# Kernel tuning notes

Hardware: AMD Instinct MI355X
Metric: run time of the kernel (lower is better)

## Reference

```python
import jax, jax.numpy as jnp
import numpy as np

B, T, Hs, Ws, D, NH, NKV = 2, 8, 16, 16, 1024, 16, 4
HD = D // NH  # 64
EPS = 1e-6
THETA = 10000.0


def setup_inputs() -> dict:
    key = jax.random.key(0)
    ks = jax.random.split(key, 6)
    N = T * Hs * Ws
    s = 0.02
    return {
        'x': jax.random.normal(ks[0], (B, N, D), jnp.float32),
        'Wq': jax.random.normal(ks[1], (D, D), jnp.float32) * s,
        'bq': jnp.zeros((D,), jnp.float32),
        'Wk': jax.random.normal(ks[2], (D, NKV * HD), jnp.float32) * s,
        'bk': jnp.zeros((NKV * HD,), jnp.float32),
        'Wv': jax.random.normal(ks[3], (D, NKV * HD), jnp.float32) * s,
        'bv': jnp.zeros((NKV * HD,), jnp.float32),
        'Wo': jax.random.normal(ks[4], (D, D), jnp.float32) * s,
        'bo': jnp.zeros((D,), jnp.float32),
        'qn_w': jnp.ones((HD,), jnp.float32),
        'kn_w': jnp.ones((HD,), jnp.float32),
        't': T, 'h': Hs, 'w': Ws,
    }


def _rms_norm(x, w):
    # RMSNorm over last dim (head_dim), eps=1e-6, learned scale
    var = jnp.mean(jnp.square(x), axis=-1, keepdims=True)
    return x * jax.lax.rsqrt(var + EPS) * w


def _rope_cs(n, d):
    inv = 1.0 / (THETA ** (np.arange(0, d, 2, dtype=np.float32) / d))
    fr = np.arange(n, dtype=np.float32)[:, None] * inv[None, :]
    emb = np.concatenate([fr, fr], axis=-1)  # (n, d)
    return jnp.asarray(np.cos(emb)), jnp.asarray(np.sin(emb))


def _rot_half(x):
    x1, x2 = jnp.split(x, 2, axis=-1)
    return jnp.concatenate([-x2, x1], axis=-1)


def _st_rope(x, t, h, w):
    # x: (B, t, h, w, heads, hd); factored 3D RoPE on head_dim split
    d = x.shape[-1]
    if d % 3 == 0:
        dt = dh = d // 3
        dw = d - 2 * dt
    else:
        dt = d // 4
        dh = d // 4
        dw = d - dt - dh
    xt, xh, xw = jnp.split(x, [dt, dt + dh], axis=-1)

    def app(xs, n, axis_pos, dd):
        cos, sin = _rope_cs(n, dd)
        shp = [1] * 6
        shp[axis_pos] = n
        shp[-1] = dd
        cos = cos.reshape(shp)
        sin = sin.reshape(shp)
        return xs * cos + _rot_half(xs) * sin

    xt = app(xt, t, 1, dt)
    xh = app(xh, h, 2, dh)
    xw = app(xw, w, 3, dw)
    return jnp.concatenate([xt, xh, xw], axis=-1)


def reference(x, Wq, bq, Wk, bk, Wv, bv, Wo, bo, qn_w, kn_w, t, h, w):
    Bx, N, Dx = x.shape
    q = (x @ Wq + bq).reshape(Bx, N, NH, HD)
    k = (x @ Wk + bk).reshape(Bx, N, NKV, HD)
    v = (x @ Wv + bv).reshape(Bx, N, NKV, HD)
    q = _rms_norm(q, qn_w)
    k = _rms_norm(k, kn_w)
    q = _st_rope(q.reshape(Bx, t, h, w, NH, HD), t, h, w).reshape(Bx, N, NH, HD)
    k = _st_rope(k.reshape(Bx, t, h, w, NKV, HD), t, h, w).reshape(Bx, N, NKV, HD)
    g = NH // NKV
    if g > 1:  # GQA: 'b m h d -> b m (h g) d'
        k = jnp.repeat(k, g, axis=2)
        v = jnp.repeat(v, g, axis=2)
    scale = HD ** -0.5
    scores = jnp.einsum('bnhd,bmhd->bhnm', q, k) * scale  # (B,H,N,N)
    p = jax.nn.softmax(scores, axis=-1)
    out = jnp.einsum('bhnm,bmhd->bnhd', p, v).reshape(Bx, N, Dx)
    return out @ Wo + bo
```

## Files before the change

kernel.cpp:

```cpp
#include <hip/hip_runtime.h>
#include <hip/hip_bf16.h>
#include <math.h>

constexpr int B_   = 2;
constexpr int N_   = 2048;
constexpr int D_   = 1024;
constexpr int NH_  = 16;
constexpr int NKV_ = 4;
constexpr int HD_  = 64;
constexpr int BN_  = 4096;
constexpr int KVD_ = NKV_ * HD_;
constexpr float EPS_ = 1e-6f;
constexpr float THETA_ = 10000.0f;

typedef _Float16 half8v __attribute__((ext_vector_type(8)));
typedef unsigned short ushort8v __attribute__((ext_vector_type(8)));
typedef float f32x4 __attribute__((ext_vector_type(4)));

static __device__ __forceinline__ unsigned short f2h(float f) {
  union { _Float16 h; unsigned short u; } v; v.h = (_Float16)f; return v.u;
}
static __device__ __forceinline__ float h2f(unsigned short u) {
  union { unsigned short u; _Float16 h; } v; v.u = u; return (float)v.h;
}

static __device__ __forceinline__ void dma16(const unsigned short* g,
                                             unsigned short* l) {
  __builtin_amdgcn_global_load_lds(
      (const __attribute__((address_space(1))) unsigned int*)g,
      (__attribute__((address_space(3))) unsigned int*)l, 16, 0, 0);
}

static __device__ __forceinline__ void wtrans_tile(
    const float* __restrict__ W, int Nw, int K, float scale,
    unsigned short* __restrict__ WTh, unsigned short* __restrict__ WTl,
    int bx, int by, bool lo)
{
  __shared__ float tile[32][33];
  const int k0 = bx * 32, n0 = by * 32;
  const int c = threadIdx.x & 31, rb = threadIdx.x >> 5;
#pragma unroll
  for (int i = 0; i < 4; ++i) {
    const int r = rb + i * 8;
    tile[r][c] = W[(size_t)(k0 + r) * Nw + n0 + c];
  }
  __syncthreads();
#pragma unroll
  for (int i = 0; i < 4; ++i) {
    const int r = rb + i * 8;
    const float v = tile[c][r] * scale;
    const size_t o = (size_t)(n0 + r) * K + k0 + c;
    const unsigned short hi = f2h(v);
    WTh[o] = hi;
    if (lo) WTl[o] = f2h(v - h2f(hi));
  }
}

__global__ __launch_bounds__(256) void prep(
    const float* __restrict__ x,
    const float* __restrict__ Wq, const float* __restrict__ Wk,
    const float* __restrict__ Wv, const float* __restrict__ Wo,
    unsigned short* __restrict__ xh,
    unsigned short* __restrict__ WqT, unsigned short* __restrict__ WkT,
    unsigned short* __restrict__ WvT,
    unsigned short* __restrict__ WoTh, unsigned short* __restrict__ WoTl)
{
  const int bid = blockIdx.x;
  if (bid < 2048) {
    const int i = (bid * 256 + threadIdx.x) * 8;
    const float4 v0 = *(const float4*)(x + i);
    const float4 v1 = *(const float4*)(x + i + 4);
    ushort8v o;
    o[0] = f2h(v0.x); o[1] = f2h(v0.y); o[2] = f2h(v0.z); o[3] = f2h(v0.w);
    o[4] = f2h(v1.x); o[5] = f2h(v1.y); o[6] = f2h(v1.z); o[7] = f2h(v1.w);
    *(ushort8v*)(xh + i) = o;
  } else if (bid < 3072) {
    const int l = bid - 2048;
    wtrans_tile(Wq, D_, D_, 1.0f, WqT, nullptr, l & 31, l >> 5, false);
  } else if (bid < 3328) {
    const int l = bid - 3072;
    wtrans_tile(Wk, KVD_, D_, 1.0f, WkT, nullptr, l & 31, l >> 5, false);
  } else if (bid < 3584) {
    const int l = bid - 3328;
    wtrans_tile(Wv, KVD_, D_, 1.0f, WvT, nullptr, l & 31, l >> 5, false);
  } else {
    const int l = bid - 3584;
    wtrans_tile(Wo, D_, D_, 64.0f, WoTh, WoTl, l & 31, l >> 5, true);
  }
}

__global__ __launch_bounds__(256) void gemm_qkv(
    const unsigned short* __restrict__ xh,
    const unsigned short* __restrict__ WqT, const unsigned short* __restrict__ WkT,
    const unsigned short* __restrict__ WvT,
    const float* __restrict__ bq, const float* __restrict__ bk, const float* __restrict__ bv,
    const float* __restrict__ qn, const float* __restrict__ kn,
    unsigned short* __restrict__ qv, unsigned short* __restrict__ kv,
    unsigned short* __restrict__ vv)
{
  __shared__ unsigned short As[128 * 64];
  __shared__ unsigned short Bs[64 * 64];

  const int y = blockIdx.y;
  const unsigned short* wt; const float* bias; unsigned short* outp; int opitch, col0, mode;
  if (y < 16)      { wt = WqT + (size_t)y * 64 * D_;        bias = bq + y * 64;        outp = qv; opitch = D_;   col0 = y * 64;        mode = 0; }
  else if (y < 20) { wt = WkT + (size_t)(y - 16) * 64 * D_; bias = bk + (y - 16) * 64; outp = kv; opitch = KVD_; col0 = (y - 16) * 64; mode = 1; }
  else             { wt = WvT + (size_t)(y - 20) * 64 * D_; bias = bv + (y - 20) * 64; outp = vv; opitch = KVD_; col0 = (y - 20) * 64; mode = 2; }

  const int bm = blockIdx.x * 128;
  const int tid = threadIdx.x;
  const int w = tid >> 6, lane = tid & 63, quad = lane >> 4, l16 = lane & 15;
  const int lr = lane >> 3;
  const int gc = (lane & 7) ^ lr;
  const int sw = l16 & 7;

  const unsigned short* gA = xh + (size_t)(bm + w * 8 + lr) * D_ + gc * 8;
  const unsigned short* gB = wt + (size_t)(w * 8 + lr) * D_ + gc * 8;

  f32x4 acc[2][4];
#pragma unroll
  for (int i = 0; i < 2; ++i)
#pragma unroll
    for (int j = 0; j < 4; ++j) acc[i][j] = (f32x4){0.f, 0.f, 0.f, 0.f};

  for (int k0 = 0; k0 < D_; k0 += 64) {
    __syncthreads();
#pragma unroll
    for (int rd = 0; rd < 4; ++rd)
      dma16(gA + (size_t)rd * 32 * D_ + k0, &As[rd * 2048 + w * 512]);
#pragma unroll
    for (int rd = 0; rd < 2; ++rd)
      dma16(gB + (size_t)rd * 32 * D_ + k0, &Bs[rd * 2048 + w * 512]);
    __syncthreads();

#pragma unroll
    for (int kk = 0; kk < 2; ++kk) {
      half8v fa[2], fb[4];
#pragma unroll
      for (int mb = 0; mb < 2; ++mb)
        fa[mb] = *(const half8v*)&As[(w * 32 + mb * 16 + l16) * 64 + ((kk * 4 + quad) ^ sw) * 8];
#pragma unroll
      for (int nb = 0; nb < 4; ++nb)
        fb[nb] = *(const half8v*)&Bs[(nb * 16 + l16) * 64 + ((kk * 4 + quad) ^ sw) * 8];
#pragma unroll
      for (int mb = 0; mb < 2; ++mb)
#pragma unroll
        for (int nb = 0; nb < 4; ++nb)
          acc[mb][nb] = __builtin_amdgcn_mfma_f32_16x16x32_f16(fa[mb], fb[nb], acc[mb][nb], 0, 0, 0);
    }
  }

  float bsv[4];
#pragma unroll
  for (int nb = 0; nb < 4; ++nb) bsv[nb] = bias[nb * 16 + l16];

  if (mode == 2) {
#pragma unroll
    for (int mb = 0; mb < 2; ++mb)
#pragma unroll
      for (int nb = 0; nb < 4; ++nb)
#pragma unroll
        for (int r = 0; r < 4; ++r) {
          const int row = bm + w * 32 + mb * 16 + quad * 4 + r;
          outp[(size_t)row * opitch + col0 + nb * 16 + l16] = f2h(acc[mb][nb][r] + bsv[nb]);
        }
    return;
  }

  const float* nwp = (mode == 0) ? qn : kn;
  float wv[4];
#pragma unroll
  for (int nb = 0; nb < 4; ++nb) wv[nb] = nwp[nb * 16 + l16];
  const float f_th = __powf(THETA_, -(float)(l16 & 7) / 8.0f);
  const float f_w  = __powf(THETA_, -(float)l16 / 16.0f);
  const float oscale = (mode == 0) ? 0.125f : 1.0f;
  const bool first8 = (l16 & 8) == 0;

  float snw[4], csw[4];
#pragma unroll
  for (int r = 0; r < 4; ++r)
    __sincosf((float)(quad * 4 + r) * f_w, &snw[r], &csw[r]);

#pragma unroll
  for (int mb = 0; mb < 2; ++mb) {
    const int nbase = (bm + w * 32 + mb * 16) & (N_ - 1);
    float snt, cst, snh, csh;
    __sincosf((float)(nbase >> 8) * f_th, &snt, &cst);
    __sincosf((float)((nbase >> 4) & 15) * f_th, &snh, &csh);
#pragma unroll
    for (int r = 0; r < 4; ++r) {
      float v[4];
      float ss = 0.f;
#pragma unroll
      for (int nb = 0; nb < 4; ++nb) { v[nb] = acc[mb][nb][r] + bsv[nb]; ss += v[nb] * v[nb]; }
      ss += __shfl_xor(ss, 1, 64);
      ss += __shfl_xor(ss, 2, 64);
      ss += __shfl_xor(ss, 4, 64);
      ss += __shfl_xor(ss, 8, 64);
      const float rs = rsqrtf(ss * (1.0f / 64.0f) + EPS_);
#pragma unroll
      for (int nb = 0; nb < 4; ++nb) v[nb] *= rs * wv[nb];

      const float p0 = __shfl_xor(v[0], 8, 64);
      const float p1 = __shfl_xor(v[1], 8, 64);
      const float o0 = v[0] * cst + (first8 ? -p0 : p0) * snt;
      const float o1 = v[1] * csh + (first8 ? -p1 : p1) * snh;
      const float o2 = v[2] * csw[r] - v[3] * snw[r];
      const float o3 = v[3] * csw[r] + v[2] * snw[r];

      const int row = bm + w * 32 + mb * 16 + quad * 4 + r;
      const size_t ob = (size_t)row * opitch + col0 + l16;
      outp[ob]      = f2h(o0 * oscale);
      outp[ob + 16] = f2h(o1 * oscale);
      outp[ob + 32] = f2h(o2 * oscale);
      outp[ob + 48] = f2h(o3 * oscale);
    }
  }
}

__global__ __launch_bounds__(256) void gemm_o(
    const unsigned short* __restrict__ ag,
    const unsigned short* __restrict__ WTh, const unsigned short* __restrict__ WTl,
    const float* __restrict__ bo, float* __restrict__ out)
{
  __shared__ unsigned short As[128 * 64];
  __shared__ unsigned short Bh[64 * 64], Bl[64 * 64];

  const int bm = blockIdx.x * 128, bn = blockIdx.y * 64;
  const int tid = threadIdx.x;
  const int w = tid >> 6, lane = tid & 63, quad = lane >> 4, l16 = lane & 15;
  const int lr = lane >> 3;
  const int gc = (lane & 7) ^ lr;
  const int sw = l16 & 7;

  const unsigned short* gA  = ag  + (size_t)(bm + w * 8 + lr) * D_ + gc * 8;
  const unsigned short* gBh = WTh + (size_t)(bn + w * 8 + lr) * D_ + gc * 8;
  const unsigned short* gBl = WTl + (size_t)(bn + w * 8 + lr) * D_ + gc * 8;

  f32x4 acc[2][4];
#pragma unroll
  for (int i = 0; i < 2; ++i)
#pragma unroll
    for (int j = 0; j < 4; ++j) acc[i][j] = (f32x4){0.f, 0.f, 0.f, 0.f};

  for (int k0 = 0; k0 < D_; k0 += 64) {
    __syncthreads();
#pragma unroll
    for (int rd = 0; rd < 4; ++rd)
      dma16(gA + (size_t)rd * 32 * D_ + k0, &As[rd * 2048 + w * 512]);
#pragma unroll
    for (int rd = 0; rd < 2; ++rd) {
      dma16(gBh + (size_t)rd * 32 * D_ + k0, &Bh[rd * 2048 + w * 512]);
      dma16(gBl + (size_t)rd * 32 * D_ + k0, &Bl[rd * 2048 + w * 512]);
    }
    __syncthreads();

#pragma unroll
    for (int kk = 0; kk < 2; ++kk) {
      half8v fa[2], fbh[4], fbl[4];
#pragma unroll
      for (int mb = 0; mb < 2; ++mb)
        fa[mb] = *(const half8v*)&As[(w * 32 + mb * 16 + l16) * 64 + ((kk * 4 + quad) ^ sw) * 8];
#pragma unroll
      for (int nb = 0; nb < 4; ++nb) {
        const int ro = (nb * 16 + l16) * 64 + ((kk * 4 + quad) ^ sw) * 8;
        fbh[nb] = *(const half8v*)&Bh[ro];
        fbl[nb] = *(const half8v*)&Bl[ro];
      }
#pragma unroll
      for (int mb = 0; mb < 2; ++mb)
#pragma unroll
        for (int nb = 0; nb < 4; ++nb) {
          acc[mb][nb] = __builtin_amdgcn_mfma_f32_16x16x32_f16(fa[mb], fbl[nb], acc[mb][nb], 0, 0, 0);
          acc[mb][nb] = __builtin_amdgcn_mfma_f32_16x16x32_f16(fa[mb], fbh[nb], acc[mb][nb], 0, 0, 0);
        }
    }
  }

  float bsv[4];
#pragma unroll
  for (int nb = 0; nb < 4; ++nb) bsv[nb] = bo[bn + nb * 16 + l16];
#pragma unroll
  for (int mb = 0; mb < 2; ++mb)
#pragma unroll
    for (int nb = 0; nb < 4; ++nb)
#pragma unroll
      for (int r = 0; r < 4; ++r) {
        const int row = bm + w * 32 + mb * 16 + quad * 4 + r;
        const int col = bn + nb * 16 + l16;
        out[(size_t)row * D_ + col] = acc[mb][nb][r] * 0.015625f + bsv[nb];
      }
}

__global__ __launch_bounds__(256) void attn_mfma(
    const unsigned short* __restrict__ qg,
    const unsigned short* __restrict__ kg,
    const unsigned short* __restrict__ vg,
    unsigned short* __restrict__ og)
{
  __shared__ unsigned short Ks[128 * 64];
  __shared__ unsigned short Vt[64][136];
  __shared__ unsigned short Pw[4][32][72];

  const int bid = blockIdx.x;
  const int qt  = bid & 15;
  const int h   = (bid >> 4) & 15;
  const int b   = bid >> 8;
  const int kvh = h >> 2;

  const int tid  = threadIdx.x;
  const int w    = tid >> 6;
  const int lane = tid & 63;
  const int quad = lane >> 4;
  const int l16  = lane & 15;
  const int lr = lane >> 3;
  const int gc = (lane & 7) ^ lr;
  const int sw = l16 & 7;

  half8v aq[2][2];
#pragma unroll
  for (int qb = 0; qb < 2; ++qb) {
    const int qrow = qt * 128 + w * 32 + qb * 16 + l16;
    const unsigned short* qptr =
        qg + ((size_t)(b * N_ + qrow) * D_) + h * HD_ + quad * 8;
    aq[qb][0] = *(const half8v*)(qptr);
    aq[qb][1] = *(const half8v*)(qptr + 32);
  }

  f32x4 o[2][4];
  float lrow[2][4];
#pragma unroll
  for (int qb = 0; qb < 2; ++qb)
#pragma unroll
    for (int i = 0; i < 4; ++i) { o[qb][i] = (f32x4){0.f, 0.f, 0.f, 0.f}; lrow[qb][i] = 0.f; }

  const unsigned short* gK =
      kg + ((size_t)(b * N_) + w * 8 + lr) * KVD_ + kvh * HD_ + gc * 8;
  const int vj = tid & 15;
  const int vh = (tid >> 4) & 1;
  const int vs = tid >> 5;

  for (int kt = 0; kt < 16; ++kt) {
    const int kbase = kt * 128;
    __syncthreads();
    {
#pragma unroll
      for (int rd = 0; rd < 4; ++rd)
        dma16(gK + (size_t)(kbase + rd * 32) * KVD_, &Ks[rd * 2048 + w * 512]);
#pragma unroll
      for (int hh = 0; hh < 2; ++hh) {
        const unsigned short* v1 =
            vg + (size_t)(b * N_ + kbase + hh * 64 + vj + 32 * vh) * KVD_ + kvh * HD_ + 8 * vs;
        const ushort8v va = *(const ushort8v*)(v1);
        const ushort8v vb8 = *(const ushort8v*)(v1 + 16 * KVD_);
        const int vcol = hh * 64 + 4 * vj + 2 * vh;
#pragma unroll
        for (int i = 0; i < 8; ++i)
          *(unsigned int*)&Vt[8 * vs + i][vcol] =
              (unsigned int)va[i] | ((unsigned int)vb8[i] << 16);
      }
    }
    __syncthreads();

#pragma unroll
    for (int hh = 0; hh < 2; ++hh) {
      f32x4 s[2][4];
#pragma unroll
      for (int nb = 0; nb < 4; ++nb) {
        const int kr = (hh * 64 + nb * 16 + l16) * 64;
        const half8v b0 = *(const half8v*)&Ks[kr + (quad ^ sw) * 8];
        const half8v b1 = *(const half8v*)&Ks[kr + ((4 + quad) ^ sw) * 8];
#pragma unroll
        for (int qb = 0; qb < 2; ++qb) {
          f32x4 z = (f32x4){0.f, 0.f, 0.f, 0.f};
          z = __builtin_amdgcn_mfma_f32_16x16x32_f16(aq[qb][0], b0, z, 0, 0, 0);
          s[qb][nb] = __builtin_amdgcn_mfma_f32_16x16x32_f16(aq[qb][1], b1, z, 0, 0, 0);
        }
      }

#pragma unroll
      for (int qb = 0; qb < 2; ++qb)
#pragma unroll
        for (int r = 0; r < 4; ++r) {
          const float p0 = __expf(s[qb][0][r]);
          const float p1 = __expf(s[qb][1][r]);
          const float p2 = __expf(s[qb][2][r]);
          const float p3 = __expf(s[qb][3][r]);
          lrow[qb][r] += (p0 + p1) + (p2 + p3);
          uint2 u;
          u.x = (unsigned int)f2h(p0) | ((unsigned int)f2h(p1) << 16);
          u.y = (unsigned int)f2h(p2) | ((unsigned int)f2h(p3) << 16);
          *(uint2*)&Pw[w][qb * 16 + quad * 4 + r][4 * l16] = u;
        }

#pragma unroll
      for (int kc = 0; kc < 2; ++kc) {
        half8v ap[2];
#pragma unroll
        for (int qb = 0; qb < 2; ++qb)
          ap[qb] = *(const half8v*)&Pw[w][qb * 16 + l16][kc * 32 + quad * 8];
#pragma unroll
        for (int nb = 0; nb < 4; ++nb) {
          const half8v bv = *(const half8v*)&Vt[nb * 16 + l16][hh * 64 + kc * 32 + quad * 8];
#pragma unroll
          for (int qb = 0; qb < 2; ++qb)
            o[qb][nb] = __builtin_amdgcn_mfma_f32_16x16x32_f16(ap[qb], bv, o[qb][nb], 0, 0, 0);
        }
      }
    }
  }

#pragma unroll
  for (int qb = 0; qb < 2; ++qb) {
#pragma unroll
    for (int r = 0; r < 4; ++r) {
      float lr2 = lrow[qb][r];
      lr2 += __shfl_xor(lr2, 1, 64);
      lr2 += __shfl_xor(lr2, 2, 64);
      lr2 += __shfl_xor(lr2, 4, 64);
      lr2 += __shfl_xor(lr2, 8, 64);
      lrow[qb][r] = 1.0f / lr2;
    }
    const size_t obase =
        ((size_t)(b * N_ + qt * 128 + w * 32 + qb * 16 + quad * 4) * D_) +
        h * HD_ + l16;
#pragma unroll
    for (int r = 0; r < 4; ++r)
#pragma unroll
      for (int nb = 0; nb < 4; ++nb)
        og[obase + (size_t)r * D_ + nb * 16] = f2h(o[qb][nb][r] * lrow[qb][r]);
  }
}

extern "C" void kernel_launch(void* const* d_in, const int* in_sizes, int n_in,
                              void* d_out, int out_size, void* d_ws, size_t ws_size,
                              hipStream_t stream) {
  const float* x  = (const float*)d_in[0];
  const float* Wq = (const float*)d_in[1];
  const float* bq = (const float*)d_in[2];
  const float* Wk = (const float*)d_in[3];
  const float* bk = (const float*)d_in[4];
  const float* Wv = (const float*)d_in[5];
  const float* bv = (const float*)d_in[6];
  const float* Wo = (const float*)d_in[7];
  const float* bo = (const float*)d_in[8];
  const float* qn = (const float*)d_in[9];
  const float* kn = (const float*)d_in[10];
  float* out = (float*)d_out;

  const size_t M4 = (size_t)BN_ * D_;
  const size_t M1 = (size_t)BN_ * KVD_;
  unsigned short* xh  = (unsigned short*)d_ws;
  unsigned short* qv  = xh + M4;
  unsigned short* kv  = qv + M4;
  unsigned short* vv  = kv + M1;
  unsigned short* WqT = vv + M1;
  unsigned short* WkT = WqT + (size_t)D_ * D_;
  unsigned short* WvT = WkT + (size_t)D_ * KVD_;
  unsigned short* WoTh = WvT + (size_t)D_ * KVD_;
  unsigned short* WoTl = WoTh + (size_t)D_ * D_;
  unsigned short* og  = xh;

  const dim3 blk(256);

  prep<<<dim3(4608), blk, 0, stream>>>(x, Wq, Wk, Wv, Wo, xh, WqT, WkT, WvT, WoTh, WoTl);

  gemm_qkv<<<dim3(32, 24), blk, 0, stream>>>(xh, WqT, WkT, WvT, bq, bk, bv, qn, kn, qv, kv, vv);

  attn_mfma<<<dim3(B_ * NH_ * (N_ / 128)), blk, 0, stream>>>(qv, kv, vv, og);

  gemm_o<<<dim3(32, 16), blk, 0, stream>>>(og, WoTh, WoTl, bo, out);
}
```

Baseline: 196.4 us.

## Use 8 waves per attention block, prefetch V into registers, use exp2

The attention kernel moves from 4 waves handling 32 query rows each to 8 waves handling 16 rows each, which raises wave-level parallelism per block and cuts per-thread register state. The V tile for the next iteration is now loaded into registers ahead of time, so global load latency overlaps with compute, and the K DMA is spread across the 8 waves. The softmax switches from exp to exp2, with log2(e) folded into the Q output scale in the QKV GEMM. The trade-off is that each K/V tile in LDS feeds fewer MFMAs per wave and 512-thread blocks synchronise more threads at each barrier.

Measured after the change: 189.5 us. 3.5% less time.

```diff
diff --git a/kernel.cpp b/kernel.cpp
--- a/kernel.cpp
+++ b/kernel.cpp
@@ -12,8 +12,10 @@
 constexpr int KVD_ = NKV_ * HD_;
 constexpr float EPS_ = 1e-6f;
 constexpr float THETA_ = 10000.0f;
+constexpr float LOG2E_ = 1.4426950408889634f;
 
 typedef _Float16 half8v __attribute__((ext_vector_type(8)));
+typedef _Float16 half2v __attribute__((ext_vector_type(2)));
 typedef unsigned short ushort8v __attribute__((ext_vector_type(8)));
 typedef float f32x4 __attribute__((ext_vector_type(4)));
 
@@ -23,6 +25,12 @@
 static __device__ __forceinline__ float h2f(unsigned short u) {
   union { unsigned short u; _Float16 h; } v; v.u = u; return (float)v.h;
 }
+
+#if __has_builtin(__builtin_amdgcn_exp2f)
+#define EXP2F(x) __builtin_amdgcn_exp2f(x)
+#else
+#define EXP2F(x) __expf((x) * 0.6931471805599453f)
+#endif
 
 static __device__ __forceinline__ void dma16(const unsigned short* g,
                                              unsigned short* l) {
@@ -173,7 +181,7 @@
   for (int nb = 0; nb < 4; ++nb) wv[nb] = nwp[nb * 16 + l16];
   const float f_th = __powf(THETA_, -(float)(l16 & 7) / 8.0f);
   const float f_w  = __powf(THETA_, -(float)l16 / 16.0f);
-  const float oscale = (mode == 0) ? 0.125f : 1.0f;
+  const float oscale = (mode == 0) ? 0.125f * LOG2E_ : 1.0f;
   const bool first8 = (l16 & 8) == 0;
 
   float snw[4], csw[4];
@@ -292,7 +300,7 @@
       }
 }
 
-__global__ __launch_bounds__(256) void attn_mfma(
+__global__ __launch_bounds__(512, 4) void attn_mfma(
     const unsigned short* __restrict__ qg,
     const unsigned short* __restrict__ kg,
     const unsigned short* __restrict__ vg,
@@ -300,7 +308,7 @@
 {
   __shared__ unsigned short Ks[128 * 64];
   __shared__ unsigned short Vt[64][136];
-  __shared__ unsigned short Pw[4][32][72];
+  __shared__ unsigned short Pw[8][16][72];
 
   const int bid = blockIdx.x;
   const int qt  = bid & 15;
@@ -317,119 +325,107 @@
   const int gc = (lane & 7) ^ lr;
   const int sw = l16 & 7;
 
-  half8v aq[2][2];
-#pragma unroll
-  for (int qb = 0; qb < 2; ++qb) {
-    const int qrow = qt * 128 + w * 32 + qb * 16 + l16;
+  half8v aq[2];
+  {
+    const int qrow = qt * 128 + w * 16 + l16;
     const unsigned short* qptr =
         qg + ((size_t)(b * N_ + qrow) * D_) + h * HD_ + quad * 8;
-    aq[qb][0] = *(const half8v*)(qptr);
-    aq[qb][1] = *(const half8v*)(qptr + 32);
-  }
-
-  f32x4 o[2][4];
-  float lrow[2][4];
-#pragma unroll
-  for (int qb = 0; qb < 2; ++qb)
-#pragma unroll
-    for (int i = 0; i < 4; ++i) { o[qb][i] = (f32x4){0.f, 0.f, 0.f, 0.f}; lrow[qb][i] = 0.f; }
+    aq[0] = *(const half8v*)(qptr);
+    aq[1] = *(const half8v*)(qptr + 32);
+  }
+
+  f32x4 o[4];
+  float lrow[4];
+#pragma unroll
+  for (int i = 0; i < 4; ++i) { o[i] = (f32x4){0.f, 0.f, 0.f, 0.f}; lrow[i] = 0.f; }
 
   const unsigned short* gK =
       kg + ((size_t)(b * N_) + w * 8 + lr) * KVD_ + kvh * HD_ + gc * 8;
-  const int vj = tid & 15;
-  const int vh = (tid >> 4) & 1;
-  const int vs = tid >> 5;
+
+  const int vj  = tid & 15;
+  const int vh  = (tid >> 4) & 1;
+  const int vs  = (tid >> 5) & 7;
+  const int vhh = tid >> 8;
+  const int vcol = vhh * 64 + 4 * vj + 2 * vh;
+  const unsigned short* gV =
+      vg + (size_t)(b * N_ + vhh * 64 + vj + 32 * vh) * KVD_ + kvh * HD_ + 8 * vs;
+
+  ushort8v va  = *(const ushort8v*)(gV);
+  ushort8v vb8 = *(const ushort8v*)(gV + 16 * KVD_);
 
   for (int kt = 0; kt < 16; ++kt) {
-    const int kbase = kt * 128;
-    __syncthreads();
-    {
-#pragma unroll
-      for (int rd = 0; rd < 4; ++rd)
-        dma16(gK + (size_t)(kbase + rd * 32) * KVD_, &Ks[rd * 2048 + w * 512]);
-#pragma unroll
-      for (int hh = 0; hh < 2; ++hh) {
-        const unsigned short* v1 =
-            vg + (size_t)(b * N_ + kbase + hh * 64 + vj + 32 * vh) * KVD_ + kvh * HD_ + 8 * vs;
-        const ushort8v va = *(const ushort8v*)(v1);
-        const ushort8v vb8 = *(const ushort8v*)(v1 + 16 * KVD_);
-        const int vcol = hh * 64 + 4 * vj + 2 * vh;
-#pragma unroll
-        for (int i = 0; i < 8; ++i)
-          *(unsigned int*)&Vt[8 * vs + i][vcol] =
-              (unsigned int)va[i] | ((unsigned int)vb8[i] << 16);
-      }
+    __syncthreads();
+#pragma unroll
+    for (int rd = 0; rd < 2; ++rd)
+      dma16(gK + (size_t)(kt * 128 + rd * 64) * KVD_, &Ks[rd * 4096 + w * 512]);
+#pragma unroll
+    for (int i = 0; i < 8; ++i)
+      *(unsigned int*)&Vt[8 * vs + i][vcol] =
+          (unsigned int)va[i] | ((unsigned int)vb8[i] << 16);
+    if (kt < 15) {
+      const unsigned short* p = gV + (size_t)(kt + 1) * 128 * KVD_;
+      va  = *(const ushort8v*)(p);
+      vb8 = *(const ushort8v*)(p + 16 * KVD_);
     }
     __syncthreads();
 
 #pragma unroll
     for (int hh = 0; hh < 2; ++hh) {
-      f32x4 s[2][4];
+      f32x4 s[4];
 #pragma unroll
       for (int nb = 0; nb < 4; ++nb) {
         const int kr = (hh * 64 + nb * 16 + l16) * 64;
         const half8v b0 = *(const half8v*)&Ks[kr + (quad ^ sw) * 8];
         const half8v b1 = *(const half8v*)&Ks[kr + ((4 + quad) ^ sw) * 8];
-#pragma unroll
-        for (int qb = 0; qb < 2; ++qb) {
-          f32x4 z = (f32x4){0.f, 0.f, 0.f, 0.f};
-          z = __builtin_amdgcn_mfma_f32_16x16x32_f16(aq[qb][0], b0, z, 0, 0, 0);
-          s[qb][nb] = __builtin_amdgcn_mfma_f32_16x16x32_f16(aq[qb][1], b1, z, 0, 0, 0);
+        f32x4 z = (f32x4){0.f, 0.f, 0.f, 0.f};
+        z = __builtin_amdgcn_mfma_f32_16x16x32_f16(aq[0], b0, z, 0, 0, 0);
+        s[nb] = __builtin_amdgcn_mfma_f32_16x16x32_f16(aq[1], b1, z, 0, 0, 0);
+      }
+
+#pragma unroll
+      for (int r = 0; r < 4; ++r) {
+        const float p0 = EXP2F(s[0][r]);
+        const float p1 = EXP2F(s[1][r]);
+        const float p2 = EXP2F(s[2][r]);
+        const float p3 = EXP2F(s[3][r]);
+        lrow[r] += (p0 + p1) + (p2 + p3);
+        half2v h01, h23;
+        h01[0] = (_Float16)p0; h01[1] = (_Float16)p1;
+        h23[0] = (_Float16)p2; h23[1] = (_Float16)p3;
+        uint2 u;
+        u.x = __builtin_bit_cast(unsigned int, h01);
+        u.y = __builtin_bit_cast(unsigned int, h23);
+        *(uint2*)&Pw[w][quad * 4 + r][4 * l16] = u;
+      }
+
+#pragma unroll
+      for (int kc = 0; kc < 2; ++kc) {
+        const half8v ap = *(const half8v*)&Pw[w][l16][kc * 32 + quad * 8];
+#pragma unroll
+        for (int nb = 0; nb < 4; ++nb) {
+          const half8v bv = *(const half8v*)&Vt[nb * 16 + l16][hh * 64 + kc * 32 + quad * 8];
+          o[nb] = __builtin_amdgcn_mfma_f32_16x16x32_f16(ap, bv, o[nb], 0, 0, 0);
         }
       }
-
-#pragma unroll
-      for (int qb = 0; qb < 2; ++qb)
-#pragma unroll
-        for (int r = 0; r < 4; ++r) {
-          const float p0 = __expf(s[qb][0][r]);
-          const float p1 = __expf(s[qb][1][r]);
-          const float p2 = __expf(s[qb][2][r]);
-          const float p3 = __expf(s[qb][3][r]);
-          lrow[qb][r] += (p0 + p1) + (p2 + p3);
-          uint2 u;
-          u.x = (unsigned int)f2h(p0) | ((unsigned int)f2h(p1) << 16);
-          u.y = (unsigned int)f2h(p2) | ((unsigned int)f2h(p3) << 16);
-          *(uint2*)&Pw[w][qb * 16 + quad * 4 + r][4 * l16] = u;
-        }
-
-#pragma unroll
-      for (int kc = 0; kc < 2; ++kc) {
-        half8v ap[2];
-#pragma unroll
-        for (int qb = 0; qb < 2; ++qb)
-          ap[qb] = *(const half8v*)&Pw[w][qb * 16 + l16][kc * 32 + quad * 8];
-#pragma unroll
-        for (int nb = 0; nb < 4; ++nb) {
-          const half8v bv = *(const half8v*)&Vt[nb * 16 + l16][hh * 64 + kc * 32 + quad * 8];
-#pragma unroll
-          for (int qb = 0; qb < 2; ++qb)
-            o[qb][nb] = __builtin_amdgcn_mfma_f32_16x16x32_f16(ap[qb], bv, o[qb][nb], 0, 0, 0);
-        }
-      }
-    }
-  }
-
-#pragma unroll
-  for (int qb = 0; qb < 2; ++qb) {
-#pragma unroll
-    for (int r = 0; r < 4; ++r) {
-      float lr2 = lrow[qb][r];
-      lr2 += __shfl_xor(lr2, 1, 64);
-      lr2 += __shfl_xor(lr2, 2, 64);
-      lr2 += __shfl_xor(lr2, 4, 64);
-      lr2 += __shfl_xor(lr2, 8, 64);
-      lrow[qb][r] = 1.0f / lr2;
-    }
-    const size_t obase =
-        ((size_t)(b * N_ + qt * 128 + w * 32 + qb * 16 + quad * 4) * D_) +
-        h * HD_ + l16;
-#pragma unroll
-    for (int r = 0; r < 4; ++r)
-#pragma unroll
-      for (int nb = 0; nb < 4; ++nb)
-        og[obase + (size_t)r * D_ + nb * 16] = f2h(o[qb][nb][r] * lrow[qb][r]);
-  }
+    }
+  }
+
+#pragma unroll
+  for (int r = 0; r < 4; ++r) {
+    float lr2 = lrow[r];
+    lr2 += __shfl_xor(lr2, 1, 64);
+    lr2 += __shfl_xor(lr2, 2, 64);
+    lr2 += __shfl_xor(lr2, 4, 64);
+    lr2 += __shfl_xor(lr2, 8, 64);
+    lrow[r] = 1.0f / lr2;
+  }
+  const size_t obase =
+      ((size_t)(b * N_ + qt * 128 + w * 16 + quad * 4) * D_) + h * HD_ + l16;
+#pragma unroll
+  for (int r = 0; r < 4; ++r)
+#pragma unroll
+    for (int nb = 0; nb < 4; ++nb)
+      og[obase + (size_t)r * D_ + nb * 16] = f2h(o[nb][r] * lrow[r]);
 }
 
 extern "C" void kernel_launch(void* const* d_in, const int* in_sizes, int n_in,
@@ -467,7 +463,7 @@
 
   gemm_qkv<<<dim3(32, 24), blk, 0, stream>>>(xh, WqT, WkT, WvT, bq, bk, bv, qn, kn, qv, kv, vv);
 
-  attn_mfma<<<dim3(B_ * NH_ * (N_ / 128)), blk, 0, stream>>>(qv, kv, vv, og);
+  attn_mfma<<<dim3(B_ * NH_ * (N_ / 128)), dim3(512), 0, stream>>>(qv, kv, vv, og);
 
   gemm_o<<<dim3(32, 16), blk, 0, stream>>>(og, WoTh, WoTl, bo, out);
 }
```

## Widen attention blocks to 512 threads, prefetch V, use exp2 softmax

Applied to the files above, without the earlier changes.

The attention kernel now runs 8 waves per block over 256 query rows. Each K/V tile loaded into shared memory is therefore reused by twice as many queries, which halves the grid and the K/V traffic per query. V for the next tile is prefetched into registers during the current iteration to hide global load latency. Q is pre-scaled by log2(e) so the softmax can use the native exp2 instruction, and the fp16 packing uses vector casts. The risks are lower occupancy from larger blocks and higher register pressure from the prefetch registers.

Measured after the change: 188.1 us. 1.04x faster.

```diff
diff --git a/kernel.cpp b/kernel.cpp
--- a/kernel.cpp
+++ b/kernel.cpp
@@ -12,8 +12,10 @@
 constexpr int KVD_ = NKV_ * HD_;
 constexpr float EPS_ = 1e-6f;
 constexpr float THETA_ = 10000.0f;
+constexpr float LOG2E_ = 1.4426950408889634f;
 
 typedef _Float16 half8v __attribute__((ext_vector_type(8)));
+typedef _Float16 half2v __attribute__((ext_vector_type(2)));
 typedef unsigned short ushort8v __attribute__((ext_vector_type(8)));
 typedef float f32x4 __attribute__((ext_vector_type(4)));
 
@@ -23,6 +25,12 @@
 static __device__ __forceinline__ float h2f(unsigned short u) {
   union { unsigned short u; _Float16 h; } v; v.u = u; return (float)v.h;
 }
+
+#if __has_builtin(__builtin_amdgcn_exp2f)
+#define EXP2F(x) __builtin_amdgcn_exp2f(x)
+#else
+#define EXP2F(x) __expf((x) * 0.6931471805599453f)
+#endif
 
 static __device__ __forceinline__ void dma16(const unsigned short* g,
                                              unsigned short* l) {
@@ -173,7 +181,7 @@
   for (int nb = 0; nb < 4; ++nb) wv[nb] = nwp[nb * 16 + l16];
   const float f_th = __powf(THETA_, -(float)(l16 & 7) / 8.0f);
   const float f_w  = __powf(THETA_, -(float)l16 / 16.0f);
-  const float oscale = (mode == 0) ? 0.125f : 1.0f;
+  const float oscale = (mode == 0) ? 0.125f * LOG2E_ : 1.0f;
   const bool first8 = (l16 & 8) == 0;
 
   float snw[4], csw[4];
@@ -292,7 +300,7 @@
       }
 }
 
-__global__ __launch_bounds__(256) void attn_mfma(
+__global__ __launch_bounds__(512, 2) void attn_mfma(
     const unsigned short* __restrict__ qg,
     const unsigned short* __restrict__ kg,
     const unsigned short* __restrict__ vg,
@@ -300,12 +308,12 @@
 {
   __shared__ unsigned short Ks[128 * 64];
   __shared__ unsigned short Vt[64][136];
-  __shared__ unsigned short Pw[4][32][72];
+  __shared__ unsigned short Pw[8][32][72];
 
   const int bid = blockIdx.x;
-  const int qt  = bid & 15;
-  const int h   = (bid >> 4) & 15;
-  const int b   = bid >> 8;
+  const int qt  = bid & 7;
+  const int h   = (bid >> 3) & 15;
+  const int b   = bid >> 7;
   const int kvh = h >> 2;
 
   const int tid  = threadIdx.x;
@@ -320,7 +328,7 @@
   half8v aq[2][2];
 #pragma unroll
   for (int qb = 0; qb < 2; ++qb) {
-    const int qrow = qt * 128 + w * 32 + qb * 16 + l16;
+    const int qrow = qt * 256 + w * 32 + qb * 16 + l16;
     const unsigned short* qptr =
         qg + ((size_t)(b * N_ + qrow) * D_) + h * HD_ + quad * 8;
     aq[qb][0] = *(const half8v*)(qptr);
@@ -336,31 +344,35 @@
 
   const unsigned short* gK =
       kg + ((size_t)(b * N_) + w * 8 + lr) * KVD_ + kvh * HD_ + gc * 8;
-  const int vj = tid & 15;
-  const int vh = (tid >> 4) & 1;
-  const int vs = tid >> 5;
+
+  const int vj  = tid & 15;
+  const int vh  = (tid >> 4) & 1;
+  const int vs  = (tid >> 5) & 7;
+  const int vhh = tid >> 8;
+  const int vcol = vhh * 64 + 4 * vj + 2 * vh;
+  const unsigned short* gV =
+      vg + (size_t)(b * N_ + vhh * 64 + vj + 32 * vh) * KVD_ + kvh * HD_ + 8 * vs;
+
+  ushort8v va  = *(const ushort8v*)(gV);
+  ushort8v vb8 = *(const ushort8v*)(gV + 16 * KVD_);
 
   for (int kt = 0; kt < 16; ++kt) {
-    const int kbase = kt * 128;
-    __syncthreads();
-    {
-#pragma unroll
-      for (int rd = 0; rd < 4; ++rd)
-        dma16(gK + (size_t)(kbase + rd * 32) * KVD_, &Ks[rd * 2048 + w * 512]);
-#pragma unroll
-      for (int hh = 0; hh < 2; ++hh) {
-        const unsigned short* v1 =
-            vg + (size_t)(b * N_ + kbase + hh * 64 + vj + 32 * vh) * KVD_ + kvh * HD_ + 8 * vs;
-        const ushort8v va = *(const ushort8v*)(v1);
-        const ushort8v vb8 = *(const ushort8v*)(v1 + 16 * KVD_);
-        const int vcol = hh * 64 + 4 * vj + 2 * vh;
-#pragma unroll
-        for (int i = 0; i < 8; ++i)
-          *(unsigned int*)&Vt[8 * vs + i][vcol] =
-              (unsigned int)va[i] | ((unsigned int)vb8[i] << 16);
-      }
-    }
-    __syncthreads();
+    __syncthreads();
+    ushort8v na, nb8;
+    if (kt < 15) {
+      const unsigned short* p = gV + (size_t)(kt + 1) * 128 * KVD_;
+      na  = *(const ushort8v*)(p);
+      nb8 = *(const ushort8v*)(p + 16 * KVD_);
+    }
+#pragma unroll
+    for (int rd = 0; rd < 2; ++rd)
+      dma16(gK + (size_t)(kt * 128 + rd * 64) * KVD_, &Ks[rd * 4096 + w * 512]);
+#pragma unroll
+    for (int i = 0; i < 8; ++i)
+      *(unsigned int*)&Vt[8 * vs + i][vcol] =
+          (unsigned int)va[i] | ((unsigned int)vb8[i] << 16);
+    __syncthreads();
+    if (kt < 15) { va = na; vb8 = nb8; }
 
 #pragma unroll
     for (int hh = 0; hh < 2; ++hh) {
@@ -382,14 +394,17 @@
       for (int qb = 0; qb < 2; ++qb)
 #pragma unroll
         for (int r = 0; r < 4; ++r) {
-          const float p0 = __expf(s[qb][0][r]);
-          const float p1 = __expf(s[qb][1][r]);
-          const float p2 = __expf(s[qb][2][r]);
-          const float p3 = __expf(s[qb][3][r]);
+          const float p0 = EXP2F(s[qb][0][r]);
+          const float p1 = EXP2F(s[qb][1][r]);
+          const float p2 = EXP2F(s[qb][2][r]);
+          const float p3 = EXP2F(s[qb][3][r]);
           lrow[qb][r] += (p0 + p1) + (p2 + p3);
+          half2v h01, h23;
+          h01[0] = (_Float16)p0; h01[1] = (_Float16)p1;
+          h23[0] = (_Float16)p2; h23[1] = (_Float16)p3;
           uint2 u;
-          u.x = (unsigned int)f2h(p0) | ((unsigned int)f2h(p1) << 16);
-          u.y = (unsigned int)f2h(p2) | ((unsigned int)f2h(p3) << 16);
+          u.x = __builtin_bit_cast(unsigned int, h01);
+          u.y = __builtin_bit_cast(unsigned int, h23);
           *(uint2*)&Pw[w][qb * 16 + quad * 4 + r][4 * l16] = u;
         }
 
@@ -422,7 +437,7 @@
       lrow[qb][r] = 1.0f / lr2;
     }
     const size_t obase =
-        ((size_t)(b * N_ + qt * 128 + w * 32 + qb * 16 + quad * 4) * D_) +
+        ((size_t)(b * N_ + qt * 256 + w * 32 + qb * 16 + quad * 4) * D_) +
         h * HD_ + l16;
 #pragma unroll
     for (int r = 0; r < 4; ++r)
@@ -467,7 +482,7 @@
 
   gemm_qkv<<<dim3(32, 24), blk, 0, stream>>>(xh, WqT, WkT, WvT, bq, bk, bv, qn, kn, qv, kv, vv);
 
-  attn_mfma<<<dim3(B_ * NH_ * (N_ / 128)), blk, 0, stream>>>(qv, kv, vv, og);
+  attn_mfma<<<dim3(B_ * NH_ * (N_ / 256)), dim3(512), 0, stream>>>(qv, kv, vv, og);
 
   gemm_o<<<dim3(32, 16), blk, 0, stream>>>(og, WoTh, WoTl, bo, out);
 }
```

## Double-buffer K/V tiles, keep P in registers via transposed MFMA, use exp2

Applied to the files above, without the earlier changes.

Attention now double-buffers K and V tiles in shared memory, prefetching the next tile and holding V two tiles ahead in registers, so each iteration needs one barrier instead of two. Swapping the MFMA operand order (computing S^T) lets each lane hold a full row of probabilities in registers, which removes the per-warp P round trip through shared memory. The log2(e) factor is folded into the Q scale so exp2 can be used, and the attention kernel declares a two-blocks-per-CU launch bound. In exchange it uses more LDS and registers, and the V store layout and output mapping are rearranged to match the transposed fragments.

Measured after the change: 179.3 us. 8.7% less time.

```diff
diff --git a/kernel.cpp b/kernel.cpp
--- a/kernel.cpp
+++ b/kernel.cpp
@@ -12,8 +12,11 @@
 constexpr int KVD_ = NKV_ * HD_;
 constexpr float EPS_ = 1e-6f;
 constexpr float THETA_ = 10000.0f;
+constexpr float LOG2E_ = 1.4426950408889634f;
 
 typedef _Float16 half8v __attribute__((ext_vector_type(8)));
+typedef _Float16 half4v __attribute__((ext_vector_type(4)));
+typedef _Float16 half2v __attribute__((ext_vector_type(2)));
 typedef unsigned short ushort8v __attribute__((ext_vector_type(8)));
 typedef float f32x4 __attribute__((ext_vector_type(4)));
 
@@ -23,6 +26,12 @@
 static __device__ __forceinline__ float h2f(unsigned short u) {
   union { unsigned short u; _Float16 h; } v; v.u = u; return (float)v.h;
 }
+
+#if __has_builtin(__builtin_amdgcn_exp2f)
+#define EXP2F(x) __builtin_amdgcn_exp2f(x)
+#else
+#define EXP2F(x) __expf((x) * 0.6931471805599453f)
+#endif
 
 static __device__ __forceinline__ void dma16(const unsigned short* g,
                                              unsigned short* l) {
@@ -173,7 +182,7 @@
   for (int nb = 0; nb < 4; ++nb) wv[nb] = nwp[nb * 16 + l16];
   const float f_th = __powf(THETA_, -(float)(l16 & 7) / 8.0f);
   const float f_w  = __powf(THETA_, -(float)l16 / 16.0f);
-  const float oscale = (mode == 0) ? 0.125f : 1.0f;
+  const float oscale = (mode == 0) ? 0.125f * LOG2E_ : 1.0f;
   const bool first8 = (l16 & 8) == 0;
 
   float snw[4], csw[4];
@@ -292,15 +301,14 @@
       }
 }
 
-__global__ __launch_bounds__(256) void attn_mfma(
+__global__ __launch_bounds__(256, 2) void attn_mfma(
     const unsigned short* __restrict__ qg,
     const unsigned short* __restrict__ kg,
     const unsigned short* __restrict__ vg,
     unsigned short* __restrict__ og)
 {
-  __shared__ unsigned short Ks[128 * 64];
-  __shared__ unsigned short Vt[64][136];
-  __shared__ unsigned short Pw[4][32][72];
+  __shared__ unsigned short Ks[2][128 * 64];
+  __shared__ unsigned short Vt[2][64][136];
 
   const int bid = blockIdx.x;
   const int qt  = bid & 15;
@@ -327,40 +335,69 @@
     aq[qb][1] = *(const half8v*)(qptr + 32);
   }
 
-  f32x4 o[2][4];
-  float lrow[2][4];
+  f32x4 o_[2][4];
+  float lrow[2] = {0.f, 0.f};
 #pragma unroll
   for (int qb = 0; qb < 2; ++qb)
 #pragma unroll
-    for (int i = 0; i < 4; ++i) { o[qb][i] = (f32x4){0.f, 0.f, 0.f, 0.f}; lrow[qb][i] = 0.f; }
+    for (int i = 0; i < 4; ++i) o_[qb][i] = (f32x4){0.f, 0.f, 0.f, 0.f};
 
   const unsigned short* gK =
       kg + ((size_t)(b * N_) + w * 8 + lr) * KVD_ + kvh * HD_ + gc * 8;
+
   const int vj = tid & 15;
   const int vh = (tid >> 4) & 1;
-  const int vs = tid >> 5;
+  const int vs = (tid >> 5) & 7;
+  const int vcol = vh * 32 + ((vj >> 1) & 3) * 8 + ((vj >> 3) & 1) * 4 + 2 * (vj & 1);
+  const unsigned short* gV =
+      vg + (size_t)(b * N_ + 2 * vj + 32 * vh) * KVD_ + kvh * HD_ + 8 * vs;
+
+#pragma unroll
+  for (int rd = 0; rd < 4; ++rd)
+    dma16(gK + (size_t)(rd * 32) * KVD_, &Ks[0][rd * 2048 + w * 512]);
+  ushort8v va[2][2];
+#pragma unroll
+  for (int hh = 0; hh < 2; ++hh) {
+    const unsigned short* p = gV + (size_t)(hh * 64) * KVD_;
+    va[hh][0] = *(const ushort8v*)(p);
+    va[hh][1] = *(const ushort8v*)(p + KVD_);
+  }
+#pragma unroll
+  for (int hh = 0; hh < 2; ++hh)
+#pragma unroll
+    for (int i = 0; i < 8; ++i)
+      *(unsigned int*)&Vt[0][8 * vs + i][hh * 64 + vcol] =
+          (unsigned int)va[hh][0][i] | ((unsigned int)va[hh][1][i] << 16);
+#pragma unroll
+  for (int hh = 0; hh < 2; ++hh) {
+    const unsigned short* p = gV + (size_t)(128 + hh * 64) * KVD_;
+    va[hh][0] = *(const ushort8v*)(p);
+    va[hh][1] = *(const ushort8v*)(p + KVD_);
+  }
+  __syncthreads();
 
   for (int kt = 0; kt < 16; ++kt) {
-    const int kbase = kt * 128;
-    __syncthreads();
-    {
+    const int cur = kt & 1;
+    if (kt < 15) {
 #pragma unroll
       for (int rd = 0; rd < 4; ++rd)
-        dma16(gK + (size_t)(kbase + rd * 32) * KVD_, &Ks[rd * 2048 + w * 512]);
-#pragma unroll
-      for (int hh = 0; hh < 2; ++hh) {
-        const unsigned short* v1 =
-            vg + (size_t)(b * N_ + kbase + hh * 64 + vj + 32 * vh) * KVD_ + kvh * HD_ + 8 * vs;
-        const ushort8v va = *(const ushort8v*)(v1);
-        const ushort8v vb8 = *(const ushort8v*)(v1 + 16 * KVD_);
-        const int vcol = hh * 64 + 4 * vj + 2 * vh;
+        dma16(gK + (size_t)((kt + 1) * 128 + rd * 32) * KVD_,
+              &Ks[cur ^ 1][rd * 2048 + w * 512]);
+#pragma unroll
+      for (int hh = 0; hh < 2; ++hh)
 #pragma unroll
         for (int i = 0; i < 8; ++i)
-          *(unsigned int*)&Vt[8 * vs + i][vcol] =
-              (unsigned int)va[i] | ((unsigned int)vb8[i] << 16);
+          *(unsigned int*)&Vt[cur ^ 1][8 * vs + i][hh * 64 + vcol] =
+              (unsigned int)va[hh][0][i] | ((unsigned int)va[hh][1][i] << 16);
+      if (kt < 14) {
+#pragma unroll
+        for (int hh = 0; hh < 2; ++hh) {
+          const unsigned short* p = gV + (size_t)((kt + 2) * 128 + hh * 64) * KVD_;
+          va[hh][0] = *(const ushort8v*)(p);
+          va[hh][1] = *(const ushort8v*)(p + KVD_);
+        }
       }
     }
-    __syncthreads();
 
 #pragma unroll
     for (int hh = 0; hh < 2; ++hh) {
@@ -368,67 +405,65 @@
 #pragma unroll
       for (int nb = 0; nb < 4; ++nb) {
         const int kr = (hh * 64 + nb * 16 + l16) * 64;
-        const half8v b0 = *(const half8v*)&Ks[kr + (quad ^ sw) * 8];
-        const half8v b1 = *(const half8v*)&Ks[kr + ((4 + quad) ^ sw) * 8];
+        const half8v b0 = *(const half8v*)&Ks[cur][kr + (quad ^ sw) * 8];
+        const half8v b1 = *(const half8v*)&Ks[cur][kr + ((4 + quad) ^ sw) * 8];
 #pragma unroll
         for (int qb = 0; qb < 2; ++qb) {
           f32x4 z = (f32x4){0.f, 0.f, 0.f, 0.f};
-          z = __builtin_amdgcn_mfma_f32_16x16x32_f16(aq[qb][0], b0, z, 0, 0, 0);
-          s[qb][nb] = __builtin_amdgcn_mfma_f32_16x16x32_f16(aq[qb][1], b1, z, 0, 0, 0);
+          z = __builtin_amdgcn_mfma_f32_16x16x32_f16(b0, aq[qb][0], z, 0, 0, 0);
+          s[qb][nb] = __builtin_amdgcn_mfma_f32_16x16x32_f16(b1, aq[qb][1], z, 0, 0, 0);
         }
       }
 
-#pragma unroll
-      for (int qb = 0; qb < 2; ++qb)
-#pragma unroll
-        for (int r = 0; r < 4; ++r) {
-          const float p0 = __expf(s[qb][0][r]);
-          const float p1 = __expf(s[qb][1][r]);
-          const float p2 = __expf(s[qb][2][r]);
-          const float p3 = __expf(s[qb][3][r]);
-          lrow[qb][r] += (p0 + p1) + (p2 + p3);
-          uint2 u;
-          u.x = (unsigned int)f2h(p0) | ((unsigned int)f2h(p1) << 16);
-          u.y = (unsigned int)f2h(p2) | ((unsigned int)f2h(p3) << 16);
-          *(uint2*)&Pw[w][qb * 16 + quad * 4 + r][4 * l16] = u;
+      half8v pf[2][2];
+#pragma unroll
+      for (int qb = 0; qb < 2; ++qb) {
+        float ls = 0.f;
+#pragma unroll
+        for (int nb = 0; nb < 4; ++nb) {
+          const float p0 = EXP2F(s[qb][nb][0]);
+          const float p1 = EXP2F(s[qb][nb][1]);
+          const float p2 = EXP2F(s[qb][nb][2]);
+          const float p3 = EXP2F(s[qb][nb][3]);
+          ls += (p0 + p1) + (p2 + p3);
+          const int kc = nb >> 1, jo = (nb & 1) * 4;
+          pf[qb][kc][jo + 0] = (_Float16)p0;
+          pf[qb][kc][jo + 1] = (_Float16)p1;
+          pf[qb][kc][jo + 2] = (_Float16)p2;
+          pf[qb][kc][jo + 3] = (_Float16)p3;
         }
-
-#pragma unroll
-      for (int kc = 0; kc < 2; ++kc) {
-        half8v ap[2];
-#pragma unroll
-        for (int qb = 0; qb < 2; ++qb)
-          ap[qb] = *(const half8v*)&Pw[w][qb * 16 + l16][kc * 32 + quad * 8];
+        lrow[qb] += ls;
+      }
+
+#pragma unroll
+      for (int kc = 0; kc < 2; ++kc)
 #pragma unroll
         for (int nb = 0; nb < 4; ++nb) {
-          const half8v bv = *(const half8v*)&Vt[nb * 16 + l16][hh * 64 + kc * 32 + quad * 8];
+          const half8v bv =
+              *(const half8v*)&Vt[cur][nb * 16 + l16][hh * 64 + kc * 32 + quad * 8];
 #pragma unroll
           for (int qb = 0; qb < 2; ++qb)
-            o[qb][nb] = __builtin_amdgcn_mfma_f32_16x16x32_f16(ap[qb], bv, o[qb][nb], 0, 0, 0);
+            o_[qb][nb] = __builtin_amdgcn_mfma_f32_16x16x32_f16(bv, pf[qb][kc], o_[qb][nb], 0, 0, 0);
         }
-      }
-    }
+    }
+    __syncthreads();
   }
 
 #pragma unroll
   for (int qb = 0; qb < 2; ++qb) {
-#pragma unroll
-    for (int r = 0; r < 4; ++r) {
-      float lr2 = lrow[qb][r];
-      lr2 += __shfl_xor(lr2, 1, 64);
-      lr2 += __shfl_xor(lr2, 2, 64);
-      lr2 += __shfl_xor(lr2, 4, 64);
-      lr2 += __shfl_xor(lr2, 8, 64);
-      lrow[qb][r] = 1.0f / lr2;
-    }
-    const size_t obase =
-        ((size_t)(b * N_ + qt * 128 + w * 32 + qb * 16 + quad * 4) * D_) +
-        h * HD_ + l16;
-#pragma unroll
-    for (int r = 0; r < 4; ++r)
-#pragma unroll
-      for (int nb = 0; nb < 4; ++nb)
-        og[obase + (size_t)r * D_ + nb * 16] = f2h(o[qb][nb][r] * lrow[qb][r]);
+    float l = lrow[qb];
+    l += __shfl_xor(l, 16, 64);
+    l += __shfl_xor(l, 32, 64);
+    const float inv = 1.0f / l;
+    const int qrow = qt * 128 + w * 32 + qb * 16 + l16;
+    const size_t base = (size_t)(b * N_ + qrow) * D_ + h * HD_;
+#pragma unroll
+    for (int nb = 0; nb < 4; ++nb) {
+      half4v pk;
+#pragma unroll
+      for (int r = 0; r < 4; ++r) pk[r] = (_Float16)(o_[qb][nb][r] * inv);
+      *(half4v*)&og[base + nb * 16 + quad * 4] = pk;
+    }
   }
 }
 
```
